# Optimization experiments

Measured on AMD Instinct MI355X. Metric: run time of the kernel, lower is better.

The kernel has to match this reference:

```python
import jax, jax.numpy as jnp
import numpy as np

B, T, F, H = 512, 64, 256, 1024


def _uniform(key, shape, fan_in):
    stv = 1.0 / np.sqrt(fan_in)
    return jax.random.uniform(key, shape, jnp.float32, -stv, stv)


def setup_inputs() -> dict:
    key = jax.random.key(0)
    ks = jax.random.split(key, 20)
    x = jax.random.normal(ks[0], (B, T, F), jnp.float32)
    mask = (jax.random.uniform(ks[1], (B, T, F)) < 0.8).astype(jnp.float32)
    deltas = jax.random.uniform(ks[2], (B, T, F), jnp.float32) * 5.0
    h0 = jnp.zeros((B, H), jnp.float32)
    return {
        "x": x, "mask": mask, "deltas": deltas, "h0": h0,
        # temp_decay_h: Decay(F -> H), non-diag
        "Wdh": _uniform(ks[3], (H, F), F), "bdh": _uniform(ks[4], (H,), F),
        # temp_decay_x: Decay(F -> F), diag (weight masked with identity)
        "Wdx": _uniform(ks[5], (F, F), F), "bdx": _uniform(ks[6], (F,), F),
        # hist: Linear(H -> F)
        "Wh": _uniform(ks[7], (F, H), H), "bh": _uniform(ks[8], (F,), H),
        "Wfr": _uniform(ks[9], (F, F), F), "bfr": _uniform(ks[10], (F,), F),
        # weight_combine: Linear(2F -> F)
        "Wwc": _uniform(ks[11], (F, 2 * F), 2 * F), "bwc": _uniform(ks[12], (F,), 2 * F),
        # GRUCell(2F, H)
        "Wih": _uniform(ks[13], (3 * H, 2 * F), 2 * F), "bih": _uniform(ks[14], (3 * H,), H),
        "Whh": _uniform(ks[15], (3 * H, H), H), "bhh": _uniform(ks[16], (3 * H,), H),
    }


def _forward(x, mask, deltas, h0, Wdh, bdh, Wdx, bdx, Wh, bh, Wfr, bfr, Wwc, bwc, Wih, bih, Whh, bhh):
    f = x.shape[-1]
    eye = jnp.eye(f, dtype=x.dtype)
    Wdx_diag = Wdx * eye              # diag Decay keeps only diagonal weights
    Wfr_off = Wfr * (1.0 - eye)

    def step(h, xs):
        x_t, m_t, d_t = xs            # each [B, F]
        gamma_h = jnp.exp(-jax.nn.relu(d_t @ Wdh.T + bdh))   # [B, H]
        h = h * gamma_h
        x_h = h @ Wh.T + bh                                   # [B, F]
        x_r = m_t * x_t + (1.0 - m_t) * x_h
        xu = x_r @ Wfr_off.T + bfr
        gamma_x = jnp.exp(-jax.nn.relu(d_t @ Wdx_diag.T + bdx))
        beta = jnp.concatenate([gamma_x, m_t], axis=1) @ Wwc.T + bwc
        x_comb = beta * xu + (1.0 - beta) * x_h
        # MAE on observed entries
        loss_t = jnp.sum(jnp.abs(x_comb - x_t) * m_t) / (jnp.sum(m_t) + 1e-12)
        x_imp_t = m_t * x_t + (1.0 - m_t) * x_comb
        rnn_in = jnp.concatenate([x_imp_t, m_t], axis=1)      # [B, 2F]
        gi = rnn_in @ Wih.T + bih                             # [B, 3H]
        gh = h @ Whh.T + bhh
        i_r, i_z, i_n = jnp.split(gi, 3, axis=1)
        h_r, h_z, h_n = jnp.split(gh, 3, axis=1)
        r = jax.nn.sigmoid(i_r + h_r)
        z = jax.nn.sigmoid(i_z + h_z)
        n = jnp.tanh(i_n + r * h_n)
        h_new = (1.0 - z) * n + z * h
        return h_new, (x_imp_t, x_comb, loss_t)

    xs = (jnp.swapaxes(x, 0, 1), jnp.swapaxes(mask, 0, 1), jnp.swapaxes(deltas, 0, 1))
    h_fin, (imp_t, rec_t, losses) = jax.lax.scan(step, h0, xs)
    x_imp = jnp.swapaxes(imp_t, 0, 1)          # [B, T, F]
    reconstruction = jnp.swapaxes(rec_t, 0, 1) # [B, T, F]
    x_loss = jnp.sum(losses)
    kl_loss = jnp.zeros((), x.dtype)           # non-bayesian path
    return x_imp, reconstruction, h_fin, x_loss, kl_loss


def reference(x, mask, deltas, h0, Wdh, bdh, Wdx, bdx, Wh, bh, Wfr, bfr, Wwc, bwc, Wih, bih, Whh, bhh):
    return _forward(x, mask, deltas, h0, Wdh, bdh, Wdx, bdx, Wh, bh, Wfr, bfr, Wwc, bwc, Wih, bih, Whh, bhh)
```

## Files before the change

### kernel.cpp

```cpp
#include <hip/hip_runtime.h>
#include <hip/hip_bf16.h>

typedef unsigned short u16;
typedef unsigned int u32;
typedef __attribute__((ext_vector_type(4))) float f32x4;
typedef __attribute__((ext_vector_type(8))) short s16x8;

#define OREC 8388608
#define OH 16777216
#define OLOSS 17301504

__device__ __forceinline__ float bf2f(u16 u) {
    union { u32 i; float f; } v; v.i = ((u32)u) << 16; return v.f;
}
__device__ __forceinline__ u16 f2bf(float f) {
    union { float f; u32 i; } v; v.f = f;
    u32 i = v.i;
    u32 r = i + 0x7FFFu + ((i >> 16) & 1u);
    return (u16)(r >> 16);
}
__device__ __forceinline__ float ldin(const void* p, int i, int bf) {
    return bf ? bf2f(((const u16*)p)[i]) : ((const float*)p)[i];
}
__device__ __forceinline__ void stout(void* p, int i, float v, int bf) {
    if (bf) ((u16*)p)[i] = f2bf(v); else ((float*)p)[i] = v;
}

#define ZACC(A) do { \
    _Pragma("unroll") for (int zi = 0; zi < 2; ++zi) \
    _Pragma("unroll") for (int zj = 0; zj < 2; ++zj) \
    _Pragma("unroll") for (int zq = 0; zq < 4; ++zq) A[zi][zj][zq] = 0.f; \
} while (0)

__device__ __forceinline__ void stage_tile(const u16* __restrict__ src, int ld, int row0, int k0,
                                           u16* lds) {
    int t = threadIdx.x;
    int row = t >> 2, seg = t & 3;
    const u16* g = src + (size_t)(row0 + row) * ld + k0 + (seg << 3);
    uint4 v = *(const uint4*)g;
    *(uint4*)&lds[(row << 5) + ((seg ^ (row & 3)) << 3)] = v;
}

__device__ __forceinline__ void gemm_loop(const u16* __restrict__ A, int lda,
                                          const u16* __restrict__ W, int ldw,
                                          int K, int m0, int n0,
                                          u16* lA, u16* lB, f32x4 acc[2][2]) {
    int lane = threadIdx.x & 63;
    int wid = threadIdx.x >> 6;
    int wr = wid >> 1, wc = wid & 1;
    int lrow = lane & 15, lseg = lane >> 4;
    int sw = (lseg ^ (lrow & 3)) << 3;
    for (int k0 = 0; k0 < K; k0 += 32) {
        __syncthreads();
        stage_tile(A, lda, m0, k0, lA);
        stage_tile(W, ldw, n0, k0, lB);
        __syncthreads();
        s16x8 af[2], bg[2];
#pragma unroll
        for (int i = 0; i < 2; i++) {
            int r = (wr << 5) + (i << 4) + lrow;
            af[i] = *(const s16x8*)&lA[(r << 5) + sw];
            int c = (wc << 5) + (i << 4) + lrow;
            bg[i] = *(const s16x8*)&lB[(c << 5) + sw];
        }
#pragma unroll
        for (int i = 0; i < 2; i++)
#pragma unroll
            for (int j = 0; j < 2; j++)
                acc[i][j] = __builtin_amdgcn_mfma_f32_16x16x32_bf16(af[i], bg[j], acc[i][j], 0, 0, 0);
    }
}

__global__ void k_zero(int* flag, float* lossN, float* lossD) {
    if (threadIdx.x == 0) *flag = 0;
    if (threadIdx.x < 64) { lossN[threadIdx.x] = 0.f; lossD[threadIdx.x] = 0.f; }
}

__global__ void k_detect(const u32* __restrict__ w, int* flag) {
    int gid = blockIdx.x * 256 + threadIdx.x;
    int found = 0;
    for (int i = gid; i < (1 << 20); i += 65536) {
        if ((w[i] & 0xFFFFu) == 0x3F80u) found = 1;
    }
    if (found) atomicOr(flag, 1);
}

__global__ void k_cvt_bf(const void* __restrict__ src, u16* __restrict__ dst, int n,
                         const int* __restrict__ flagp) {
    int bf = *flagp;
    for (int i = blockIdx.x * 256 + threadIdx.x; i < n; i += gridDim.x * 256)
        dst[i] = bf ? ((const u16*)src)[i] : f2bf(((const float*)src)[i]);
}

__global__ void k_packW2(const void* __restrict__ Wih, const void* __restrict__ Whh,
                         u16* __restrict__ W2B, const int* __restrict__ flagp) {
    int bf = *flagp;
    int c = blockIdx.x;
    int k0 = threadIdx.x;
#pragma unroll
    for (int j = 0; j < 6; ++j) {
        int k = k0 + (j << 8);
        float v = (k < 512) ? ldin(Wih, c * 512 + k, bf)
                            : ldin(Whh, c * 1024 + (k - 512), bf);
        W2B[(size_t)c * 1536 + k] = f2bf(v);
    }
}

__global__ void k_cvt_biases(const void* __restrict__ bdh, const void* __restrict__ bdx,
                             const void* __restrict__ bh, const void* __restrict__ bfr,
                             const void* __restrict__ bwc, const void* __restrict__ bih,
                             const void* __restrict__ bhh, float* __restrict__ dst,
                             const int* __restrict__ flagp) {
    int bf = *flagp;
    int i = blockIdx.x * 256 + threadIdx.x;
    const void* src; int off;
    if (i < 1024) { src = bdh; off = 0; }
    else if (i < 1280) { src = bdx; off = 1024; }
    else if (i < 1536) { src = bh; off = 1280; }
    else if (i < 1792) { src = bfr; off = 1536; }
    else if (i < 2048) { src = bwc; off = 1792; }
    else if (i < 5120) { src = bih; off = 2048; }
    else { src = bhh; off = 5120; }
    dst[i] = ldin(src, i - off, bf);
}

__global__ void k_fixup(u16* __restrict__ WfrB, float* __restrict__ wdxd,
                        const void* __restrict__ Wdx, const int* __restrict__ flagp) {
    int f = threadIdx.x;
    int bf = *flagp;
    WfrB[f * 256 + f] = 0;
    wdxd[f] = ldin(Wdx, f * 257, bf);
}

__global__ void k_pack(const void* __restrict__ deltas, const void* __restrict__ mask,
                       const int* __restrict__ flagp,
                       const float* __restrict__ wdxd, const float* __restrict__ bdx,
                       u16* __restrict__ dbf_all, u16* __restrict__ A2_all) {
    int bf = *flagp;
    for (int idx = blockIdx.x * 256 + threadIdx.x; idx < 8388608; idx += gridDim.x * 256) {
        int f = idx & 255;
        int bt = idx >> 8;
        int b = bt >> 6, t = bt & 63;
        float d = ldin(deltas, idx, bf);
        float m = ldin(mask, idx, bf);
        int r = t * 512 + b;
        dbf_all[(r << 8) + f] = f2bf(d);
        float gx = expf(-fmaxf(d * wdxd[f] + bdx[f], 0.f));
        A2_all[(r << 9) + f] = f2bf(gx);
        A2_all[(r << 9) + 256 + f] = f2bf(m);
    }
}

__global__ __launch_bounds__(256) void k_gammaH(const u16* __restrict__ dbf_all,
                                                const u16* __restrict__ WdhB,
                                                const float* __restrict__ bdh,
                                                u16* __restrict__ gammaH) {
    __shared__ u16 lA[2048], lB[2048];
    int m0 = blockIdx.x << 6, n0 = blockIdx.y << 6;
    f32x4 acc[2][2]; ZACC(acc);
    gemm_loop(dbf_all, 256, WdhB, 256, 256, m0, n0, lA, lB, acc);
    int lane = threadIdx.x & 63, wid = threadIdx.x >> 6;
    int wr = wid >> 1, wc = wid & 1;
    int rq = (lane >> 4) << 2, cc = lane & 15;
#pragma unroll
    for (int i = 0; i < 2; i++)
#pragma unroll
        for (int j = 0; j < 2; j++)
#pragma unroll
            for (int q = 0; q < 4; q++) {
                int gr = m0 + (wr << 5) + (i << 4) + rq + q;
                int gc = n0 + (wc << 5) + (j << 4) + cc;
                gammaH[((size_t)gr << 10) + gc] = f2bf(expf(-fmaxf(acc[i][j][q] + bdh[gc], 0.f)));
            }
}

__global__ __launch_bounds__(256) void k_beta(const u16* __restrict__ A2_all,
                                              const u16* __restrict__ WwcB,
                                              const float* __restrict__ bwc,
                                              float* __restrict__ beta_all) {
    __shared__ u16 lA[2048], lB[2048];
    int m0 = blockIdx.x << 6, n0 = blockIdx.y << 6;
    f32x4 acc[2][2]; ZACC(acc);
    gemm_loop(A2_all, 512, WwcB, 512, 512, m0, n0, lA, lB, acc);
    int lane = threadIdx.x & 63, wid = threadIdx.x >> 6;
    int wr = wid >> 1, wc = wid & 1;
    int rq = (lane >> 4) << 2, cc = lane & 15;
#pragma unroll
    for (int i = 0; i < 2; i++)
#pragma unroll
        for (int j = 0; j < 2; j++)
#pragma unroll
            for (int q = 0; q < 4; q++) {
                int gr = m0 + (wr << 5) + (i << 4) + rq + q;
                int gc = n0 + (wc << 5) + (j << 4) + cc;
                beta_all[((size_t)gr << 8) + gc] = acc[i][j][q] + bwc[gc];
            }
}

__global__ void k_hinit(const void* __restrict__ h0, const int* __restrict__ flagp,
                        const u16* __restrict__ gammaH, u16* __restrict__ A3x) {
    int bf = *flagp;
    int i = blockIdx.x * 256 + threadIdx.x;
    float g = bf2f(gammaH[i]);
    float hv = ldin(h0, i, bf) * g;
    int r = i >> 10, c = i & 1023;
    A3x[(size_t)r * 2560 + 512 + c] = f2bf(hv);
}

__global__ __launch_bounds__(512) void k_step1(
    u16* __restrict__ A3x, float* __restrict__ pbuf,
    const u16* __restrict__ WhB, const u16* __restrict__ WfrB,
    const u16* __restrict__ W2B,
    const float* __restrict__ biases, const float* __restrict__ beta_all,
    const void* __restrict__ x, const void* __restrict__ mask,
    int t, const int* __restrict__ flagp,
    void* __restrict__ out, float* __restrict__ lossN, float* __restrict__ lossD) {
    __shared__ u16 smem[20736];
    __shared__ float redN[8], redD[8];
    int tid = threadIdx.x, bid = blockIdx.x;
    int lane = tid & 63, w = tid >> 6;
    int lrow = lane & 15, lseg = lane >> 4;
    int hsel = 512 + ((t & 1) << 10);

    if (bid < 32) {
        u16* lH = smem;
        u16* lXR = smem + 16512;
        int m0 = bid << 4;
        int c0 = w << 5;
        int bf = *flagp;
        {
            int row = tid >> 5;
            int colb = (tid & 31) << 3;
            const u16* src = A3x + (size_t)(m0 + row) * 2560 + hsel;
#pragma unroll
            for (int j = 0; j < 4; ++j) {
                int off = colb + (j << 8);
                *(uint4*)&lH[row * 1032 + off] = *(const uint4*)&src[off];
            }
        }
        __syncthreads();

        f32x4 acc[2] = {};
#pragma unroll 4
        for (int k0 = 0; k0 < 1024; k0 += 32) {
            int kk = k0 + (lseg << 3);
            s16x8 a = *(const s16x8*)&lH[lrow * 1032 + kk];
#pragma unroll
            for (int j = 0; j < 2; ++j) {
                s16x8 b = *(const s16x8*)&WhB[((size_t)(c0 + (j << 4) + lrow) << 10) + kk];
                acc[j] = __builtin_amdgcn_mfma_f32_16x16x32_bf16(a, b, acc[j], 0, 0, 0);
            }
        }

        float xhr[2][4], mvr[2][4], xvr[2][4];
#pragma unroll
        for (int j = 0; j < 2; ++j) {
            int gc = c0 + (j << 4) + lrow;
            float bhc = biases[1280 + gc];
#pragma unroll
            for (int q = 0; q < 4; ++q) {
                int r = (lseg << 2) + q;
                float v = acc[j][q] + bhc;
                int gidx = ((m0 + r) << 14) + (t << 8) + gc;
                float mv = ldin(mask, gidx, bf);
                float xv = ldin(x, gidx, bf);
                xhr[j][q] = v; mvr[j][q] = mv; xvr[j][q] = xv;
                lXR[r * 264 + gc] = f2bf(mv * xv + (1.f - mv) * v);
            }
        }
        __syncthreads();

        f32x4 accF[2] = {};
#pragma unroll
        for (int k0 = 0; k0 < 256; k0 += 32) {
            int kk = k0 + (lseg << 3);
            s16x8 a = *(const s16x8*)&lXR[lrow * 264 + kk];
#pragma unroll
            for (int j = 0; j < 2; ++j) {
                s16x8 b = *(const s16x8*)&WfrB[((size_t)(c0 + (j << 4) + lrow) << 8) + kk];
                accF[j] = __builtin_amdgcn_mfma_f32_16x16x32_bf16(a, b, accF[j], 0, 0, 0);
            }
        }

        float ln = 0.f, ldn = 0.f;
#pragma unroll
        for (int j = 0; j < 2; ++j) {
            int gc = c0 + (j << 4) + lrow;
            float bfrc = biases[1536 + gc];
#pragma unroll
            for (int q = 0; q < 4; ++q) {
                int r = (lseg << 2) + q;
                int gr = m0 + r;
                float xu = accF[j][q] + bfrc;
                float beta = beta_all[(((size_t)t * 512 + gr) << 8) + gc];
                float xc = beta * xu + (1.f - beta) * xhr[j][q];
                int gidx = (gr << 14) + (t << 8) + gc;
                float mv = mvr[j][q], xv = xvr[j][q];
                stout(out, OREC + gidx, xc, bf);
                float xi = mv * xv + (1.f - mv) * xc;
                stout(out, gidx, xi, bf);
                A3x[(size_t)gr * 2560 + gc] = f2bf(xi);
                A3x[(size_t)gr * 2560 + 256 + gc] = f2bf(mv);
                ln += fabsf(xc - xv) * mv;
                ldn += mv;
            }
        }
        for (int o = 32; o > 0; o >>= 1) { ln += __shfl_down(ln, o); ldn += __shfl_down(ldn, o); }
        if (lane == 0) { redN[w] = ln; redD[w] = ldn; }
        __syncthreads();
        if (tid == 0) {
            float sn = 0.f, sd = 0.f;
#pragma unroll
            for (int i = 0; i < 8; ++i) { sn += redN[i]; sd += redD[i]; }
            atomicAdd(&lossN[t], sn);
            atomicAdd(&lossD[t], sd);
        }
    } else {
        u16* lds = smem;
        int g = bid - 32;
        int m0 = (g >> 4) << 5, n0 = (g & 15) << 6;
        int wr = w & 1, wc = w >> 1;

        int br0 = tid >> 2, sg0 = tid & 3;
        int g0 = br0 >> 6;
        const u16* Bg0 = W2B + (size_t)(g0 * 1024 + n0 + (br0 & 63)) * 1536 + 512 + (sg0 << 3);
        int isB1 = (tid < 256), isA1 = (tid >= 256 && tid < 384);
        int br1 = 128 + (tid >> 2);
        const u16* Bg1 = W2B + (size_t)(2048 + n0 + (br1 & 63)) * 1536 + 512 + (sg0 << 3);
        int ar1 = (tid - 256) >> 2, sg1 = tid & 3;
        const u16* Ag1 = A3x + (size_t)(m0 + ar1) * 2560 + hsel + (sg1 << 3);

        uint4 p0, p1;
        auto issue = [&](int it) {
            int ko = it << 5;
            p0 = *(const uint4*)(Bg0 + ko);
            if (isB1) p1 = *(const uint4*)(Bg1 + ko);
            else if (isA1) p1 = *(const uint4*)(Ag1 + ko);
        };
        auto store = [&](u16* lb) {
            *(uint4*)&lb[br0 * 40 + (sg0 << 3)] = p0;
            if (isB1) *(uint4*)&lb[br1 * 40 + (sg0 << 3)] = p1;
            else if (isA1) *(uint4*)&lb[7680 + ar1 * 40 + (sg1 << 3)] = p1;
        };

        f32x4 aR = {0.f, 0.f, 0.f, 0.f}, aZ = {0.f, 0.f, 0.f, 0.f}, aN = {0.f, 0.f, 0.f, 0.f};
        issue(0);
        store(lds);
        __syncthreads();
        int cur = 0;
#pragma unroll 1
        for (int it = 0; it < 32; ++it) {
            if (it + 1 < 32) issue(it + 1);
            u16* lc = lds + (cur ? 8960 : 0);
            s16x8 a = *(const s16x8*)&lc[7680 + ((wr << 4) + lrow) * 40 + (lseg << 3)];
            int bro = ((wc << 4) + lrow) * 40 + (lseg << 3);
            s16x8 b0 = *(const s16x8*)&lc[bro];
            aR = __builtin_amdgcn_mfma_f32_16x16x32_bf16(a, b0, aR, 0, 0, 0);
            s16x8 b1 = *(const s16x8*)&lc[2560 + bro];
            aZ = __builtin_amdgcn_mfma_f32_16x16x32_bf16(a, b1, aZ, 0, 0, 0);
            s16x8 b2 = *(const s16x8*)&lc[5120 + bro];
            aN = __builtin_amdgcn_mfma_f32_16x16x32_bf16(a, b2, aN, 0, 0, 0);
            if (it + 1 < 32) store(lds + (cur ? 0 : 8960));
            __syncthreads();
            cur ^= 1;
        }

        int colR = n0 + (wc << 4) + lrow;
#pragma unroll
        for (int q = 0; q < 4; ++q) {
            int row = m0 + (wr << 4) + (lseg << 2) + q;
            float* pr = pbuf + (size_t)row * 3072 + colR;
            pr[0] = aR[q];
            pr[1024] = aZ[q];
            pr[2048] = aN[q];
        }
    }
}

__global__ __launch_bounds__(512) void k_step2(
    u16* __restrict__ A3x, const u16* __restrict__ W2B,
    const float* __restrict__ pbuf, const float* __restrict__ biases,
    const u16* __restrict__ gammaH, int t, void* __restrict__ out,
    const int* __restrict__ flagp) {
    __shared__ u16 lds[2 * 8960];
    int tid = threadIdx.x, bid = blockIdx.x;
    int m0 = (bid >> 4) << 5, n0 = (bid & 15) << 6;
    int lane = tid & 63, w = tid >> 6;
    int wr = w & 1, wc = w >> 1;
    int lrow = lane & 15, lseg = lane >> 4;

    int br0 = tid >> 2, sg0 = tid & 3;
    int g0 = br0 >> 6;
    const u16* Bg0 = W2B + (size_t)(g0 * 1024 + n0 + (br0 & 63)) * 1536 + (sg0 << 3);
    int isB1 = (tid < 256), isA1 = (tid >= 256 && tid < 384);
    int br1 = 128 + (tid >> 2);
    const u16* Bg1 = W2B + (size_t)(2048 + n0 + (br1 & 63)) * 1536 + (sg0 << 3);
    int ar1 = (tid - 256) >> 2, sg1 = tid & 3;
    const u16* Ag1 = A3x + (size_t)(m0 + ar1) * 2560 + (sg1 << 3);

    uint4 p0, p1;
    auto issue = [&](int it) {
        int ko = it << 5;
        p0 = *(const uint4*)(Bg0 + ko);
        if (isB1) p1 = *(const uint4*)(Bg1 + ko);
        else if (isA1) p1 = *(const uint4*)(Ag1 + ko);
    };
    auto store = [&](u16* lb) {
        *(uint4*)&lb[br0 * 40 + (sg0 << 3)] = p0;
        if (isB1) *(uint4*)&lb[br1 * 40 + (sg0 << 3)] = p1;
        else if (isA1) *(uint4*)&lb[7680 + ar1 * 40 + (sg1 << 3)] = p1;
    };

    f32x4 aR = {0.f, 0.f, 0.f, 0.f}, aZ = {0.f, 0.f, 0.f, 0.f}, aN = {0.f, 0.f, 0.f, 0.f};
    issue(0);
    store(lds);
    __syncthreads();
    int cur = 0;
#pragma unroll 1
    for (int it = 0; it < 16; ++it) {
        if (it + 1 < 16) issue(it + 1);
        u16* lc = lds + (cur ? 8960 : 0);
        s16x8 a = *(const s16x8*)&lc[7680 + ((wr << 4) + lrow) * 40 + (lseg << 3)];
        int bro = ((wc << 4) + lrow) * 40 + (lseg << 3);
        s16x8 b0 = *(const s16x8*)&lc[bro];
        aR = __builtin_amdgcn_mfma_f32_16x16x32_bf16(a, b0, aR, 0, 0, 0);
        s16x8 b1 = *(const s16x8*)&lc[2560 + bro];
        aZ = __builtin_amdgcn_mfma_f32_16x16x32_bf16(a, b1, aZ, 0, 0, 0);
        s16x8 b2 = *(const s16x8*)&lc[5120 + bro];
        aN = __builtin_amdgcn_mfma_f32_16x16x32_bf16(a, b2, aN, 0, 0, 0);
        if (it + 1 < 16) store(lds + (cur ? 0 : 8960));
        __syncthreads();
        cur ^= 1;
    }

    int bf = *flagp;
    int hsel = 512 + ((t & 1) << 10);
    int nseg = 512 + (((t + 1) & 1) << 10);
    int last = (t == 63);
    int colR = n0 + (wc << 4) + lrow;
    float bRi = biases[2048 + colR] + biases[5120 + colR];
    float bZi = biases[3072 + colR] + biases[6144 + colR];
    float bNi = biases[4096 + colR];
    float bNh = biases[7168 + colR];
#pragma unroll
    for (int q = 0; q < 4; ++q) {
        int row = m0 + (wr << 4) + (lseg << 2) + q;
        const float* pr = pbuf + (size_t)row * 3072 + colR;
        float rr = 1.f / (1.f + expf(-(aR[q] + pr[0] + bRi)));
        float zz = 1.f / (1.f + expf(-(aZ[q] + pr[1024] + bZi)));
        float nn = tanhf(aN[q] + bNi + rr * (pr[2048] + bNh));
        float hp = bf2f(A3x[(size_t)row * 2560 + hsel + colR]);
        float hv = (1.f - zz) * nn + zz * hp;
        if (!last) {
            hv *= bf2f(gammaH[(((size_t)(t + 1) * 512 + row) << 10) + colR]);
            A3x[(size_t)row * 2560 + nseg + colR] = f2bf(hv);
        } else {
            stout(out, OH + (row << 10) + colR, hv, bf);
        }
    }
}

__global__ void k_loss(const float* __restrict__ lossN, const float* __restrict__ lossD,
                       void* __restrict__ out, const int* __restrict__ flagp) {
    int t = threadIdx.x;
    float v = lossN[t] / (lossD[t] + 1e-12f);
    for (int o = 32; o > 0; o >>= 1) v += __shfl_down(v, o);
    if (t == 0) {
        int bf = *flagp;
        stout(out, OLOSS, v, bf);
        stout(out, OLOSS + 1, 0.f, bf);
    }
}

extern "C" void kernel_launch(void* const* d_in, const int* in_sizes, int n_in,
                              void* d_out, int out_size, void* d_ws, size_t ws_size,
                              hipStream_t stream) {
    (void)in_sizes; (void)n_in; (void)out_size; (void)ws_size;
    const void* x = d_in[0];
    const void* mask = d_in[1];
    const void* deltas = d_in[2];
    const void* h0 = d_in[3];
    const void* Wdh = d_in[4];  const void* bdh = d_in[5];
    const void* Wdx = d_in[6];  const void* bdx = d_in[7];
    const void* Wh = d_in[8];   const void* bh = d_in[9];
    const void* Wfr = d_in[10]; const void* bfr = d_in[11];
    const void* Wwc = d_in[12]; const void* bwc = d_in[13];
    const void* Wih = d_in[14]; const void* bih = d_in[15];
    const void* Whh = d_in[16]; const void* bhh = d_in[17];

    char* cur = (char*)d_ws;
    auto carve = [&](size_t bytes) -> char* {
        char* p = cur; cur += (bytes + 255) & ~(size_t)255; return p;
    };
    int* flag = (int*)carve(sizeof(int));
    float* lossN = (float*)carve(64 * 4);
    float* lossD = (float*)carve(64 * 4);
    float* wdxd = (float*)carve(256 * 4);
    float* biasesF = (float*)carve(8192 * 4);
    u16* WdhB = (u16*)carve(262144 * 2);
    u16* WhB = (u16*)carve(262144 * 2);
    u16* WfrB = (u16*)carve(65536 * 2);
    u16* WwcB = (u16*)carve(131072 * 2);
    u16* W2B = (u16*)carve((size_t)4718592 * 2);
    u16* A3x = (u16*)carve((size_t)512 * 2560 * 2);
    float* pbuf = (float*)carve((size_t)512 * 3072 * 4);
    u16* dbf_all = (u16*)carve((size_t)8388608 * 2);
    u16* A2_all = (u16*)carve((size_t)16777216 * 2);
    u16* gammaH_all = (u16*)carve((size_t)33554432 * 2);
    float* beta_all = (float*)carve((size_t)8388608 * 4);

    float* bdhF = biasesF;
    float* bdxF = biasesF + 1024;

    k_zero<<<1, 64, 0, stream>>>(flag, lossN, lossD);
    k_detect<<<256, 256, 0, stream>>>((const u32*)mask, flag);
    k_cvt_bf<<<1024, 256, 0, stream>>>(Wdh, WdhB, 262144, flag);
    k_cvt_bf<<<1024, 256, 0, stream>>>(Wh, WhB, 262144, flag);
    k_cvt_bf<<<256, 256, 0, stream>>>(Wfr, WfrB, 65536, flag);
    k_cvt_bf<<<512, 256, 0, stream>>>(Wwc, WwcB, 131072, flag);
    k_packW2<<<3072, 256, 0, stream>>>(Wih, Whh, W2B, flag);
    k_cvt_biases<<<32, 256, 0, stream>>>(bdh, bdx, bh, bfr, bwc, bih, bhh, biasesF, flag);
    k_fixup<<<1, 256, 0, stream>>>(WfrB, wdxd, Wdx, flag);

    k_pack<<<8192, 256, 0, stream>>>(deltas, mask, flag, wdxd, bdxF, dbf_all, A2_all);
    k_gammaH<<<dim3(512, 16), 256, 0, stream>>>(dbf_all, WdhB, bdhF, gammaH_all);
    k_beta<<<dim3(512, 4), 256, 0, stream>>>(A2_all, WwcB, biasesF + 1792, beta_all);
    k_hinit<<<2048, 256, 0, stream>>>(h0, flag, gammaH_all, A3x);

    for (int t = 0; t < 64; ++t) {
        k_step1<<<288, 512, 0, stream>>>(A3x, pbuf, WhB, WfrB, W2B, biasesF, beta_all,
                                         x, mask, t, flag, d_out, lossN, lossD);
        k_step2<<<256, 512, 0, stream>>>(A3x, W2B, pbuf, biasesF, gammaH_all, t, d_out, flag);
    }
    k_loss<<<1, 64, 0, stream>>>(lossN, lossD, d_out, flag);
}
```

Before: 3.184 ms.

## Store beta, pbuf and x in bf16 time-major layout and remap n-tile order

```diff
diff --git a/kernel.cpp b/kernel.cpp
--- a/kernel.cpp
+++ b/kernel.cpp
@@ -132,10 +132,11 @@
     wdxd[f] = ldin(Wdx, f * 257, bf);
 }
 
-__global__ void k_pack(const void* __restrict__ deltas, const void* __restrict__ mask,
-                       const int* __restrict__ flagp,
+__global__ void k_pack(const void* __restrict__ x, const void* __restrict__ deltas,
+                       const void* __restrict__ mask, const int* __restrict__ flagp,
                        const float* __restrict__ wdxd, const float* __restrict__ bdx,
-                       u16* __restrict__ dbf_all, u16* __restrict__ A2_all) {
+                       u16* __restrict__ dbf_all, u16* __restrict__ A2_all,
+                       u16* __restrict__ xbf_all) {
     int bf = *flagp;
     for (int idx = blockIdx.x * 256 + threadIdx.x; idx < 8388608; idx += gridDim.x * 256) {
         int f = idx & 255;
@@ -143,8 +144,10 @@
         int b = bt >> 6, t = bt & 63;
         float d = ldin(deltas, idx, bf);
         float m = ldin(mask, idx, bf);
+        float xv = ldin(x, idx, bf);
         int r = t * 512 + b;
         dbf_all[(r << 8) + f] = f2bf(d);
+        xbf_all[(r << 8) + f] = f2bf(xv);
         float gx = expf(-fmaxf(d * wdxd[f] + bdx[f], 0.f));
         A2_all[(r << 9) + f] = f2bf(gx);
         A2_all[(r << 9) + 256 + f] = f2bf(m);
@@ -177,7 +180,7 @@
 __global__ __launch_bounds__(256) void k_beta(const u16* __restrict__ A2_all,
                                               const u16* __restrict__ WwcB,
                                               const float* __restrict__ bwc,
-                                              float* __restrict__ beta_all) {
+                                              u16* __restrict__ betaB) {
     __shared__ u16 lA[2048], lB[2048];
     int m0 = blockIdx.x << 6, n0 = blockIdx.y << 6;
     f32x4 acc[2][2]; ZACC(acc);
@@ -193,7 +196,7 @@
             for (int q = 0; q < 4; q++) {
                 int gr = m0 + (wr << 5) + (i << 4) + rq + q;
                 int gc = n0 + (wc << 5) + (j << 4) + cc;
-                beta_all[((size_t)gr << 8) + gc] = acc[i][j][q] + bwc[gc];
+                betaB[((size_t)gr << 8) + gc] = f2bf(acc[i][j][q] + bwc[gc]);
             }
 }
 
@@ -208,11 +211,11 @@
 }
 
 __global__ __launch_bounds__(512) void k_step1(
-    u16* __restrict__ A3x, float* __restrict__ pbuf,
+    u16* __restrict__ A3x, u16* __restrict__ pbufB,
     const u16* __restrict__ WhB, const u16* __restrict__ WfrB,
     const u16* __restrict__ W2B,
-    const float* __restrict__ biases, const float* __restrict__ beta_all,
-    const void* __restrict__ x, const void* __restrict__ mask,
+    const float* __restrict__ biases, const u16* __restrict__ betaB,
+    const u16* __restrict__ xbf_all, const u16* __restrict__ A2_all,
     int t, const int* __restrict__ flagp,
     void* __restrict__ out, float* __restrict__ lossN, float* __restrict__ lossD) {
     __shared__ u16 smem[20736];
@@ -260,10 +263,11 @@
 #pragma unroll
             for (int q = 0; q < 4; ++q) {
                 int r = (lseg << 2) + q;
+                int gr = m0 + r;
                 float v = acc[j][q] + bhc;
-                int gidx = ((m0 + r) << 14) + (t << 8) + gc;
-                float mv = ldin(mask, gidx, bf);
-                float xv = ldin(x, gidx, bf);
+                size_t rbase = (size_t)t * 512 + gr;
+                float mv = bf2f(A2_all[(rbase << 9) + 256 + gc]);
+                float xv = bf2f(xbf_all[(rbase << 8) + gc]);
                 xhr[j][q] = v; mvr[j][q] = mv; xvr[j][q] = xv;
                 lXR[r * 264 + gc] = f2bf(mv * xv + (1.f - mv) * v);
             }
@@ -292,7 +296,7 @@
                 int r = (lseg << 2) + q;
                 int gr = m0 + r;
                 float xu = accF[j][q] + bfrc;
-                float beta = beta_all[(((size_t)t * 512 + gr) << 8) + gc];
+                float beta = bf2f(betaB[(((size_t)t * 512 + gr) << 8) + gc]);
                 float xc = beta * xu + (1.f - beta) * xhr[j][q];
                 int gidx = (gr << 14) + (t << 8) + gc;
                 float mv = mvr[j][q], xv = xvr[j][q];
@@ -318,7 +322,8 @@
     } else {
         u16* lds = smem;
         int g = bid - 32;
-        int m0 = (g >> 4) << 5, n0 = (g & 15) << 6;
+        int nt = ((g & 7) << 1) | ((g >> 3) & 1);
+        int m0 = (g >> 4) << 5, n0 = nt << 6;
         int wr = w & 1, wc = w >> 1;
 
         int br0 = tid >> 2, sg0 = tid & 3;
@@ -369,22 +374,23 @@
 #pragma unroll
         for (int q = 0; q < 4; ++q) {
             int row = m0 + (wr << 4) + (lseg << 2) + q;
-            float* pr = pbuf + (size_t)row * 3072 + colR;
-            pr[0] = aR[q];
-            pr[1024] = aZ[q];
-            pr[2048] = aN[q];
+            size_t o = ((size_t)row << 10) + colR;
+            pbufB[o] = f2bf(aR[q]);
+            pbufB[524288 + o] = f2bf(aZ[q]);
+            pbufB[1048576 + o] = f2bf(aN[q]);
         }
     }
 }
 
 __global__ __launch_bounds__(512) void k_step2(
     u16* __restrict__ A3x, const u16* __restrict__ W2B,
-    const float* __restrict__ pbuf, const float* __restrict__ biases,
+    const u16* __restrict__ pbufB, const float* __restrict__ biases,
     const u16* __restrict__ gammaH, int t, void* __restrict__ out,
     const int* __restrict__ flagp) {
     __shared__ u16 lds[2 * 8960];
     int tid = threadIdx.x, bid = blockIdx.x;
-    int m0 = (bid >> 4) << 5, n0 = (bid & 15) << 6;
+    int nt = ((bid & 7) << 1) | ((bid >> 3) & 1);
+    int m0 = (bid >> 4) << 5, n0 = nt << 6;
     int lane = tid & 63, w = tid >> 6;
     int wr = w & 1, wc = w >> 1;
     int lrow = lane & 15, lseg = lane >> 4;
@@ -445,10 +451,10 @@
 #pragma unroll
     for (int q = 0; q < 4; ++q) {
         int row = m0 + (wr << 4) + (lseg << 2) + q;
-        const float* pr = pbuf + (size_t)row * 3072 + colR;
-        float rr = 1.f / (1.f + expf(-(aR[q] + pr[0] + bRi)));
-        float zz = 1.f / (1.f + expf(-(aZ[q] + pr[1024] + bZi)));
-        float nn = tanhf(aN[q] + bNi + rr * (pr[2048] + bNh));
+        size_t o = ((size_t)row << 10) + colR;
+        float rr = 1.f / (1.f + expf(-(aR[q] + bf2f(pbufB[o]) + bRi)));
+        float zz = 1.f / (1.f + expf(-(aZ[q] + bf2f(pbufB[524288 + o]) + bZi)));
+        float nn = tanhf(aN[q] + bNi + rr * (bf2f(pbufB[1048576 + o]) + bNh));
         float hp = bf2f(A3x[(size_t)row * 2560 + hsel + colR]);
         float hv = (1.f - zz) * nn + zz * hp;
         if (!last) {
@@ -503,11 +509,12 @@
     u16* WwcB = (u16*)carve(131072 * 2);
     u16* W2B = (u16*)carve((size_t)4718592 * 2);
     u16* A3x = (u16*)carve((size_t)512 * 2560 * 2);
-    float* pbuf = (float*)carve((size_t)512 * 3072 * 4);
+    u16* pbufB = (u16*)carve((size_t)3 * 524288 * 2);
     u16* dbf_all = (u16*)carve((size_t)8388608 * 2);
     u16* A2_all = (u16*)carve((size_t)16777216 * 2);
+    u16* xbf_all = (u16*)carve((size_t)8388608 * 2);
     u16* gammaH_all = (u16*)carve((size_t)33554432 * 2);
-    float* beta_all = (float*)carve((size_t)8388608 * 4);
+    u16* betaB = (u16*)carve((size_t)8388608 * 2);
 
     float* bdhF = biasesF;
     float* bdxF = biasesF + 1024;
@@ -522,15 +529,17 @@
     k_cvt_biases<<<32, 256, 0, stream>>>(bdh, bdx, bh, bfr, bwc, bih, bhh, biasesF, flag);
     k_fixup<<<1, 256, 0, stream>>>(WfrB, wdxd, Wdx, flag);
 
-    k_pack<<<8192, 256, 0, stream>>>(deltas, mask, flag, wdxd, bdxF, dbf_all, A2_all);
+    k_pack<<<8192, 256, 0, stream>>>(x, deltas, mask, flag, wdxd, bdxF,
+                                     dbf_all, A2_all, xbf_all);
     k_gammaH<<<dim3(512, 16), 256, 0, stream>>>(dbf_all, WdhB, bdhF, gammaH_all);
-    k_beta<<<dim3(512, 4), 256, 0, stream>>>(A2_all, WwcB, biasesF + 1792, beta_all);
+    k_beta<<<dim3(512, 4), 256, 0, stream>>>(A2_all, WwcB, biasesF + 1792, betaB);
     k_hinit<<<2048, 256, 0, stream>>>(h0, flag, gammaH_all, A3x);
 
     for (int t = 0; t < 64; ++t) {
-        k_step1<<<288, 512, 0, stream>>>(A3x, pbuf, WhB, WfrB, W2B, biasesF, beta_all,
-                                         x, mask, t, flag, d_out, lossN, lossD);
-        k_step2<<<256, 512, 0, stream>>>(A3x, W2B, pbuf, biasesF, gammaH_all, t, d_out, flag);
+        k_step1<<<288, 512, 0, stream>>>(A3x, pbufB, WhB, WfrB, W2B, biasesF, betaB,
+                                         xbf_all, A2_all, t, flag, d_out, lossN, lossD);
+        k_step2<<<256, 512, 0, stream>>>(A3x, W2B, pbufB, biasesF, gammaH_all, t,
+                                         d_out, flag);
     }
     k_loss<<<1, 64, 0, stream>>>(lossN, lossD, d_out, flag);
 }
```

Measured after the change: 2.948 ms. 7.4% less time.
